# Performance work log

Hardware: AMD Instinct MI355X
Metric: run time of the kernel (lower is better)

## Reference

```python
import jax, jax.numpy as jnp
import numpy as np

# Graph / model dims (see init_kwargs)
N = 50000          # nodes
E = 800000         # edges (before self loops)
IN, HID, OUT = 128, 64, 47
HEADS = (4, 4, 1)
SLOPE = 0.2        # PyG GATConv default negative_slope
# dropout p=0.6 in the torch module is a no-op in eval mode -> omitted


def _glorot(key, shape):
    fan_in = shape[0] if len(shape) == 2 else int(np.prod(shape))
    return jax.random.normal(key, shape, jnp.float32) / np.sqrt(fan_in)


def setup_inputs() -> dict:
    key = jax.random.key(0)
    ks = jax.random.split(key, 16)
    x = jax.random.normal(ks[0], (N, IN), jnp.float32)
    edge_index = jax.random.randint(ks[1], (2, E), 0, N)
    # layer dims: (in_dim, out_dim_per_head, heads)
    dims = [(IN, HID, HEADS[0]), (HID * HEADS[0], HID, HEADS[1]), (HID * HEADS[1], OUT, HEADS[2])]
    inp = {"x": x, "edge_index": edge_index}
    for i, (d_in, c, h) in enumerate(dims, start=1):
        inp[f"W{i}"] = _glorot(ks[3 * i], (d_in, h * c))
        inp[f"a{i}s"] = _glorot(ks[3 * i + 1], (h, c))
        inp[f"a{i}d"] = _glorot(ks[3 * i + 2], (h, c))
        inp[f"b{i}"] = jnp.zeros((h * c,), jnp.float32)
    return inp


def gat_layer(x, src, dst, W, a_s, a_d, b, h, c):
    # x: [N, d_in] -> per-head features [N, h, c]
    feat = (x @ W).reshape(N, h, c)
    # per-node attention logits [N, h]
    al_src = jnp.einsum('nhc,hc->nh', feat, a_s)
    al_dst = jnp.einsum('nhc,hc->nh', feat, a_d)
    # per-edge score, LeakyReLU (PyG: alpha = a_src[src] + a_dst[dst])
    e = jax.nn.leaky_relu(al_src[src] + al_dst[dst], SLOPE)  # [Etot, h]
    # segment softmax over incoming edges of each dst node
    emax = jax.ops.segment_max(e, dst, num_segments=N)       # [N, h]
    w = jnp.exp(e - emax[dst])
    denom = jax.ops.segment_sum(w, dst, num_segments=N)      # [N, h]
    alpha = w / denom[dst]                                   # [Etot, h]
    # weighted scatter-add aggregation
    out = jax.ops.segment_sum(alpha[:, :, None] * feat[src], dst, num_segments=N)
    return out.reshape(N, h * c) + b                         # concat heads + bias


def reference(x, edge_index, W1, a1s, a1d, b1, W2, a2s, a2d, b2, W3, a3s, a3d, b3):
    loop = jnp.arange(N, dtype=edge_index.dtype)
    src = jnp.concatenate([edge_index[0], loop])  # add_self_loops=True
    dst = jnp.concatenate([edge_index[1], loop])
    h = gat_layer(x, src, dst, W1, a1s, a1d, b1, HEADS[0], HID)
    h = jax.nn.elu(h)
    h = gat_layer(h, src, dst, W2, a2s, a2d, b2, HEADS[1], HID)
    h = jax.nn.elu(h)
    h = gat_layer(h, src, dst, W3, a3s, a3d, b3, HEADS[2], OUT)  # no elu on last layer
    return h
```

## Files before the change

kernel.cpp:

```cpp
#include <hip/hip_runtime.h>
#include <hip/hip_bf16.h>

#define NNODES 50000
#define NEDGES 800000
#define ETOT   (NNODES + NEDGES)
#define MTILES 3136
#define MPAD   (MTILES * 16)
#define NBLK   196

typedef __attribute__((ext_vector_type(8))) short short8;
typedef __attribute__((ext_vector_type(4))) float floatx4;
typedef __attribute__((ext_vector_type(2))) unsigned int uint2v;
typedef __attribute__((ext_vector_type(4))) short short4v;

__device__ __forceinline__ float bf2f(__hip_bfloat16 x) { return __bfloat162float(x); }
__device__ __forceinline__ __hip_bfloat16 f2bf(float f) { return __float2bfloat16(f); }
__device__ __forceinline__ float sane(float v, float c) {
  v = (v == v) ? v : 0.f;
  return fminf(fmaxf(v, -c), c);
}
__device__ __forceinline__ unsigned short bfbits(float f) {
  union { __hip_bfloat16 b; unsigned short u; } cv;
  cv.b = f2bf(f);
  return cv.u;
}

__global__ void zero_int_kernel(int* __restrict__ p, int n) {
  int i = blockIdx.x * blockDim.x + threadIdx.x;
  if (i < n) p[i] = 0;
}
__global__ void fill_out_kernel(float* __restrict__ o, int n, float v) {
  int i = blockIdx.x * blockDim.x + threadIdx.x;
  if (i < n) o[i] = v;
}
__global__ void split_input_kernel(const float* __restrict__ in,
                                   __hip_bfloat16* __restrict__ hi,
                                   __hip_bfloat16* __restrict__ lo) {
  int i = blockIdx.x * blockDim.x + threadIdx.x;
  if (i >= MPAD * 256) return;
  float v = (i < NNODES * 128) ? sane(in[i], 1e4f) : 0.f;
  __hip_bfloat16 h = f2bf(v);
  hi[i] = h;
  lo[i] = f2bf(v - bf2f(h));
}
__global__ void pad47_kernel(const float* __restrict__ a, const float* __restrict__ b,
                             float* __restrict__ ap, float* __restrict__ bp) {
  int i = threadIdx.x;
  ap[i] = (i < 47) ? sane(a[i], 1e4f) : 0.f;
  bp[i] = (i < 47) ? sane(b[i], 1e4f) : 0.f;
}

__global__ void degree_kernel(const int* __restrict__ ei, int* __restrict__ deg) {
  int p = blockIdx.x * blockDim.x + threadIdx.x;
  if (p >= ETOT) return;
  int dst = (p < NEDGES) ? ei[NEDGES + p] : (p - NEDGES);
  dst = min(max(dst, 0), NNODES - 1);
  atomicAdd(&deg[dst], 1);
}

__global__ __launch_bounds__(256) void block_sum_kernel(const int* __restrict__ deg,
                                                        int* __restrict__ bsum) {
  __shared__ int sh[256];
  int b = blockIdx.x, t = threadIdx.x;
  int i = b * 256 + t;
  sh[t] = (i < NNODES) ? deg[i] : 0;
  __syncthreads();
  for (int off = 128; off > 0; off >>= 1) {
    if (t < off) sh[t] += sh[t + off];
    __syncthreads();
  }
  if (t == 0) bsum[b] = sh[0];
}

__global__ __launch_bounds__(256) void scan_bsum_kernel(const int* __restrict__ bsum,
                                                        int* __restrict__ boff,
                                                        int* __restrict__ row_ptr) {
  __shared__ int sh[256];
  int t = threadIdx.x;
  int v = (t < NBLK) ? bsum[t] : 0;
  sh[t] = v;
  __syncthreads();
  for (int off = 1; off < 256; off <<= 1) {
    int u = (t >= off) ? sh[t - off] : 0;
    __syncthreads();
    sh[t] += u;
    __syncthreads();
  }
  if (t < NBLK) boff[t] = sh[t] - v;
  if (t == 255) row_ptr[NNODES] = sh[255];
}

__global__ __launch_bounds__(256) void emit_rowptr_kernel(const int* __restrict__ deg,
                                                          const int* __restrict__ boff,
                                                          int* __restrict__ row_ptr,
                                                          int* __restrict__ cursor) {
  __shared__ int sh[256];
  int b = blockIdx.x, t = threadIdx.x;
  int i = b * 256 + t;
  int d = (i < NNODES) ? deg[i] : 0;
  sh[t] = d;
  __syncthreads();
  for (int off = 1; off < 256; off <<= 1) {
    int u = (t >= off) ? sh[t - off] : 0;
    __syncthreads();
    sh[t] += u;
    __syncthreads();
  }
  if (i < NNODES) {
    int v = boff[b] + sh[t] - d;
    row_ptr[i] = v;
    cursor[i] = v;
  }
}

__global__ void scatter_kernel(const int* __restrict__ ei, int* __restrict__ cursor,
                               int* __restrict__ csr_src) {
  int p = blockIdx.x * blockDim.x + threadIdx.x;
  if (p >= ETOT) return;
  int src, dst;
  if (p < NEDGES) { src = ei[p]; dst = ei[NEDGES + p]; }
  else            { src = p - NEDGES; dst = src; }
  src = min(max(src, 0), NNODES - 1);
  dst = min(max(dst, 0), NNODES - 1);
  int pos = atomicAdd(&cursor[dst], 1);
  pos = min(max(pos, 0), ETOT - 1);
  csr_src[pos] = src;
}

__global__ void pack_w_kernel(const float* __restrict__ W,
                              __hip_bfloat16* __restrict__ Bh,
                              __hip_bfloat16* __restrict__ Bl,
                              int K, int Nreal, int Npad) {
  int idx = blockIdx.x * blockDim.x + threadIdx.x;
  if (idx >= Npad * K) return;
  int e = idx;
  int j = e & 7;    e >>= 3;
  int m = e & 15;   e >>= 4;
  int quad = e & 3; e >>= 2;
  int kch = K >> 5;
  int kk32 = e % kch;
  int nt = e / kch;
  int n = nt * 16 + m;
  int k = kk32 * 32 + quad * 8 + j;
  float v = (n < Nreal) ? sane(W[k * Nreal + n], 1e4f) : 0.f;
  __hip_bfloat16 h = f2bf(v);
  Bh[idx] = h;
  Bl[idx] = f2bf(v - bf2f(h));
}

template<int KDIM, int NOUT, int HEADS, int WAVES_N>
__global__ __launch_bounds__(256) void gemm_attn_kernel(
    const __hip_bfloat16* __restrict__ Ah, const __hip_bfloat16* __restrict__ Al,
    const __hip_bfloat16* __restrict__ Bh, const __hip_bfloat16* __restrict__ Bl,
    const float* __restrict__ asv, const float* __restrict__ adv,
    __hip_bfloat16* __restrict__ Ch, float* __restrict__ als, float* __restrict__ ald) {
  constexpr int KCH = KDIM / 32;
  constexpr int CT = (NOUT / 16) / WAVES_N;
  constexpr int RT = 4;
  constexpr int RGROUPS = 4 / WAVES_N;
  __shared__ __hip_bfloat16 sAh[2 * 64 * 32];
  __shared__ __hip_bfloat16 sAl[2 * 64 * 32];
  int wave = threadIdx.x >> 6, lane = threadIdx.x & 63;
  int wrow = wave / WAVES_N, wcol = wave % WAVES_N;
  int rt0 = (blockIdx.x * RGROUPS + wrow) * RT;
  int ct0 = wcol * CT;
  int m = lane & 15, quad = lane >> 4;

  const short8* Bph = reinterpret_cast<const short8*>(Bh);
  const short8* Bpl = reinterpret_cast<const short8*>(Bl);

  floatx4 acc[RT][CT];
#pragma unroll
  for (int rt = 0; rt < RT; ++rt)
#pragma unroll
    for (int ct = 0; ct < CT; ++ct) acc[rt][ct] = (floatx4){0.f, 0.f, 0.f, 0.f};

  int tid = threadIdx.x;
  size_t gstage = (size_t)(rt0 * 16 + (tid >> 2)) * KDIM + (tid & 3) * 8;

#pragma unroll 2
  for (int ks = 0; ks < KCH / 2; ++ks) {
    short8 a_h[RT], a_l[RT];
    if constexpr (WAVES_N == 4) {
      short8 vh0 = *reinterpret_cast<const short8*>(Ah + gstage + ks * 64);
      short8 vh1 = *reinterpret_cast<const short8*>(Ah + gstage + ks * 64 + 32);
      short8 vl0 = *reinterpret_cast<const short8*>(Al + gstage + ks * 64);
      short8 vl1 = *reinterpret_cast<const short8*>(Al + gstage + ks * 64 + 32);
      __syncthreads();
      *reinterpret_cast<short8*>(&sAh[tid * 8]) = vh0;
      *reinterpret_cast<short8*>(&sAh[2048 + tid * 8]) = vh1;
      *reinterpret_cast<short8*>(&sAl[tid * 8]) = vl0;
      *reinterpret_cast<short8*>(&sAl[2048 + tid * 8]) = vl1;
      __syncthreads();
#pragma unroll
      for (int kk0 = 0; kk0 < 2; ++kk0) {
#pragma unroll
        for (int rt = 0; rt < RT; ++rt) {
          int so = kk0 * 2048 + (rt * 16 + m) * 32 + quad * 8;
          a_h[rt] = *reinterpret_cast<const short8*>(&sAh[so]);
          a_l[rt] = *reinterpret_cast<const short8*>(&sAl[so]);
        }
        int kk = ks * 2 + kk0;
#pragma unroll
        for (int ct = 0; ct < CT; ++ct) {
          size_t o = ((size_t)(ct0 + ct) * KCH + kk) * 64 + lane;
          short8 b_h = Bph[o];
          short8 b_l = Bpl[o];
#pragma unroll
          for (int rt = 0; rt < RT; ++rt) {
            acc[rt][ct] = __builtin_amdgcn_mfma_f32_16x16x32_bf16(a_h[rt], b_h, acc[rt][ct], 0, 0, 0);
            acc[rt][ct] = __builtin_amdgcn_mfma_f32_16x16x32_bf16(a_h[rt], b_l, acc[rt][ct], 0, 0, 0);
            acc[rt][ct] = __builtin_amdgcn_mfma_f32_16x16x32_bf16(a_l[rt], b_h, acc[rt][ct], 0, 0, 0);
          }
        }
      }
    } else {
#pragma unroll
      for (int kk0 = 0; kk0 < 2; ++kk0) {
        int kk = ks * 2 + kk0;
#pragma unroll
        for (int rt = 0; rt < RT; ++rt) {
          size_t aoff = (size_t)((rt0 + rt) * 16 + m) * KDIM + kk * 32 + quad * 8;
          a_h[rt] = *reinterpret_cast<const short8*>(Ah + aoff);
          a_l[rt] = *reinterpret_cast<const short8*>(Al + aoff);
        }
#pragma unroll
        for (int ct = 0; ct < CT; ++ct) {
          size_t o = ((size_t)(ct0 + ct) * KCH + kk) * 64 + lane;
          short8 b_h = Bph[o];
          short8 b_l = Bpl[o];
#pragma unroll
          for (int rt = 0; rt < RT; ++rt) {
            acc[rt][ct] = __builtin_amdgcn_mfma_f32_16x16x32_bf16(a_h[rt], b_h, acc[rt][ct], 0, 0, 0);
            acc[rt][ct] = __builtin_amdgcn_mfma_f32_16x16x32_bf16(a_h[rt], b_l, acc[rt][ct], 0, 0, 0);
            acc[rt][ct] = __builtin_amdgcn_mfma_f32_16x16x32_bf16(a_l[rt], b_h, acc[rt][ct], 0, 0, 0);
          }
        }
      }
    }
  }

  constexpr int CPH = NOUT / HEADS;
  int head = (ct0 * 16) / CPH;
  float asl[CT], adl[CT];
#pragma unroll
  for (int ct = 0; ct < CT; ++ct) {
    asl[ct] = asv[(ct0 + ct) * 16 + m];
    adl[ct] = adv[(ct0 + ct) * 16 + m];
  }
  float ps[RT * 4], pd[RT * 4];
#pragma unroll
  for (int i = 0; i < RT * 4; ++i) { ps[i] = 0.f; pd[i] = 0.f; }
#pragma unroll
  for (int rt = 0; rt < RT; ++rt)
#pragma unroll
    for (int ct = 0; ct < CT; ++ct)
#pragma unroll
      for (int r = 0; r < 4; ++r) {
        ps[rt * 4 + r] += acc[rt][ct][r] * asl[ct];
        pd[rt * 4 + r] += acc[rt][ct][r] * adl[ct];
      }
#pragma unroll
  for (int off = 1; off < 16; off <<= 1) {
#pragma unroll
    for (int i = 0; i < RT * 4; ++i) {
      ps[i] += __shfl_xor(ps[i], off);
      pd[i] += __shfl_xor(pd[i], off);
    }
  }
  if (m == 0) {
#pragma unroll
    for (int rt = 0; rt < RT; ++rt)
#pragma unroll
      for (int r = 0; r < 4; ++r) {
        int row = (rt0 + rt) * 16 + quad * 4 + r;
        if (row < NNODES) {
          als[(size_t)row * HEADS + head] = sane(ps[rt * 4 + r], 80.f);
          ald[(size_t)row * HEADS + head] = sane(pd[rt * 4 + r], 80.f);
        }
      }
  }

#pragma unroll
  for (int rt = 0; rt < RT; ++rt)
#pragma unroll
    for (int ct = 0; ct < CT; ++ct)
#pragma unroll
      for (int r = 0; r < 4; ++r) {
        int row = (rt0 + rt) * 16 + quad * 4 + r;
        if (row < NNODES) {
          float v = sane(acc[rt][ct][r], 3e4f);
          Ch[(size_t)row * NOUT + (ct0 + ct) * 16 + m] = f2bf(v);
        }
      }
}

template<int H>
__global__ __launch_bounds__(256) void alpha_kernel(const int* __restrict__ row_ptr,
                                                    const int* __restrict__ csr_src,
                                                    const float* __restrict__ als,
                                                    const float* __restrict__ ald,
                                                    float* __restrict__ alpha) {
  int wid = threadIdx.x >> 6, lane = threadIdx.x & 63;
  int dst = blockIdx.x * 4 + wid;
  if (dst >= NNODES) return;
  int start = row_ptr[dst], end = row_ptr[dst + 1];
  int cnt = end - start;
  if (cnt <= 0) return;
  float adv[H];
#pragma unroll
  for (int h = 0; h < H; ++h) adv[h] = ald[(size_t)dst * H + h];

  if (cnt <= 64) {
    int i = start + lane;
    bool valid = lane < cnt;
    int s = valid ? min(max(csr_src[i], 0), NNODES - 1) : 0;
    float w[H];
#pragma unroll
    for (int h = 0; h < H; ++h) {
      float e = als[(size_t)s * H + h] + adv[h];
      e = e > 0.f ? e : 0.2f * e;
      e = fminf(fmaxf(e, -80.f), 80.f);
      w[h] = valid ? __expf(e) : 0.f;
    }
#pragma unroll
    for (int h = 0; h < H; ++h) {
      float v = w[h];
#pragma unroll
      for (int off = 1; off < 64; off <<= 1) v += __shfl_xor(v, off);
      float inv = 1.f / fmaxf(v, 1e-30f);
      if (valid) alpha[(size_t)i * H + h] = w[h] * inv;
    }
  } else {
    float dl[H];
#pragma unroll
    for (int h = 0; h < H; ++h) dl[h] = 0.f;
    for (int base = start; base < end; base += 64) {
      int i = base + lane;
      bool valid = i < end;
      int s = valid ? min(max(csr_src[i], 0), NNODES - 1) : 0;
#pragma unroll
      for (int h = 0; h < H; ++h) {
        float e = als[(size_t)s * H + h] + adv[h];
        e = e > 0.f ? e : 0.2f * e;
        e = fminf(fmaxf(e, -80.f), 80.f);
        float w = valid ? __expf(e) : 0.f;
        dl[h] += w;
        if (valid) alpha[(size_t)i * H + h] = w;
      }
    }
    float inv[H];
#pragma unroll
    for (int h = 0; h < H; ++h) {
      float v = dl[h];
#pragma unroll
      for (int off = 1; off < 64; off <<= 1) v += __shfl_xor(v, off);
      inv[h] = 1.f / fmaxf(v, 1e-30f);
    }
    for (int base = start; base < end; base += 64) {
      int i = base + lane;
      if (i < end)
#pragma unroll
        for (int h = 0; h < H; ++h) alpha[(size_t)i * H + h] *= inv[h];
    }
  }
}

__global__ __launch_bounds__(256) void agg_mid_kernel(const int* __restrict__ row_ptr,
                                                      const int* __restrict__ csr_src,
                                                      const __hip_bfloat16* __restrict__ Fh,
                                                      const float* __restrict__ alpha,
                                                      const float* __restrict__ bias,
                                                      __hip_bfloat16* __restrict__ Oh,
                                                      __hip_bfloat16* __restrict__ Ol) {
  int wid = threadIdx.x >> 6, lane = threadIdx.x & 63;
  int dst = blockIdx.x * 4 + wid;
  if (dst >= NNODES) return;
  int start = row_ptr[dst], end = row_ptr[dst + 1];
  int cnt = end - start;
  int head = lane >> 4;
  float a0 = 0.f, a1 = 0.f, a2 = 0.f, a3 = 0.f;
  int p = 0;
  for (; p + 3 < cnt; p += 4) {
    int e0 = start + p, e1 = e0 + 1, e2 = e0 + 2, e3 = e0 + 3;
    int s0 = csr_src[e0], s1 = csr_src[e1], s2 = csr_src[e2], s3 = csr_src[e3];
    float w0 = alpha[(size_t)e0 * 4 + head];
    float w1 = alpha[(size_t)e1 * 4 + head];
    float w2 = alpha[(size_t)e2 * 4 + head];
    float w3 = alpha[(size_t)e3 * 4 + head];
    uint2v f0 = *reinterpret_cast<const uint2v*>(Fh + (size_t)s0 * 256 + lane * 4);
    uint2v f1 = *reinterpret_cast<const uint2v*>(Fh + (size_t)s1 * 256 + lane * 4);
    uint2v f2 = *reinterpret_cast<const uint2v*>(Fh + (size_t)s2 * 256 + lane * 4);
    uint2v f3 = *reinterpret_cast<const uint2v*>(Fh + (size_t)s3 * 256 + lane * 4);
    a0 += w0 * __uint_as_float(f0.x << 16);
    a1 += w0 * __uint_as_float(f0.x & 0xffff0000u);
    a2 += w0 * __uint_as_float(f0.y << 16);
    a3 += w0 * __uint_as_float(f0.y & 0xffff0000u);
    a0 += w1 * __uint_as_float(f1.x << 16);
    a1 += w1 * __uint_as_float(f1.x & 0xffff0000u);
    a2 += w1 * __uint_as_float(f1.y << 16);
    a3 += w1 * __uint_as_float(f1.y & 0xffff0000u);
    a0 += w2 * __uint_as_float(f2.x << 16);
    a1 += w2 * __uint_as_float(f2.x & 0xffff0000u);
    a2 += w2 * __uint_as_float(f2.y << 16);
    a3 += w2 * __uint_as_float(f2.y & 0xffff0000u);
    a0 += w3 * __uint_as_float(f3.x << 16);
    a1 += w3 * __uint_as_float(f3.x & 0xffff0000u);
    a2 += w3 * __uint_as_float(f3.y << 16);
    a3 += w3 * __uint_as_float(f3.y & 0xffff0000u);
  }
  for (; p < cnt; ++p) {
    int e0 = start + p;
    int s0 = csr_src[e0];
    float w0 = alpha[(size_t)e0 * 4 + head];
    uint2v f0 = *reinterpret_cast<const uint2v*>(Fh + (size_t)s0 * 256 + lane * 4);
    a0 += w0 * __uint_as_float(f0.x << 16);
    a1 += w0 * __uint_as_float(f0.x & 0xffff0000u);
    a2 += w0 * __uint_as_float(f0.y << 16);
    a3 += w0 * __uint_as_float(f0.y & 0xffff0000u);
  }
  floatx4 bv = *reinterpret_cast<const floatx4*>(bias + lane * 4);
  float o0 = a0 + bv.x, o1 = a1 + bv.y, o2 = a2 + bv.z, o3 = a3 + bv.w;
  o0 = o0 > 0.f ? o0 : __expf(o0) - 1.f;
  o1 = o1 > 0.f ? o1 : __expf(o1) - 1.f;
  o2 = o2 > 0.f ? o2 : __expf(o2) - 1.f;
  o3 = o3 > 0.f ? o3 : __expf(o3) - 1.f;
  float h0 = bf2f(f2bf(o0)), h1 = bf2f(f2bf(o1)), h2 = bf2f(f2bf(o2)), h3 = bf2f(f2bf(o3));
  short4v hv = (short4v){(short)bfbits(o0), (short)bfbits(o1), (short)bfbits(o2), (short)bfbits(o3)};
  short4v lv = (short4v){(short)bfbits(o0 - h0), (short)bfbits(o1 - h1),
                         (short)bfbits(o2 - h2), (short)bfbits(o3 - h3)};
  *reinterpret_cast<short4v*>(Oh + (size_t)dst * 256 + lane * 4) = hv;
  *reinterpret_cast<short4v*>(Ol + (size_t)dst * 256 + lane * 4) = lv;
}

__global__ void agg_final_kernel(const int* __restrict__ row_ptr,
                                 const int* __restrict__ csr_src,
                                 const __hip_bfloat16* __restrict__ Fh,
                                 const float* __restrict__ alpha,
                                 const float* __restrict__ bias,
                                 float* __restrict__ out) {
  int wid = threadIdx.x >> 6, lane = threadIdx.x & 63;
  int dst = blockIdx.x * 4 + wid;
  if (dst >= NNODES) return;
  int start = row_ptr[dst], end = row_ptr[dst + 1];
  int cnt = end - start;
  float acc = 0.f;
  int p = 0;
  for (; p + 3 < cnt; p += 4) {
    int e0 = start + p;
    int s0 = csr_src[e0], s1 = csr_src[e0 + 1], s2 = csr_src[e0 + 2], s3 = csr_src[e0 + 3];
    float w0 = alpha[e0], w1 = alpha[e0 + 1], w2 = alpha[e0 + 2], w3 = alpha[e0 + 3];
    float f0 = bf2f(Fh[(size_t)s0 * 64 + lane]);
    float f1 = bf2f(Fh[(size_t)s1 * 64 + lane]);
    float f2 = bf2f(Fh[(size_t)s2 * 64 + lane]);
    float f3 = bf2f(Fh[(size_t)s3 * 64 + lane]);
    acc += w0 * f0 + w1 * f1 + w2 * f2 + w3 * f3;
  }
  for (; p < cnt; ++p) {
    int e0 = start + p;
    acc += alpha[e0] * bf2f(Fh[(size_t)csr_src[e0] * 64 + lane]);
  }
  if (lane < 47) out[(size_t)dst * 47 + lane] = acc + bias[lane];
}

extern "C" void kernel_launch(void* const* d_in, const int* in_sizes, int n_in,
                              void* d_out, int out_size, void* d_ws, size_t ws_size,
                              hipStream_t stream) {
  const float* x   = (const float*)d_in[0];
  const int* ei    = (const int*)d_in[1];
  const float* W1  = (const float*)d_in[2];
  const float* a1s = (const float*)d_in[3];
  const float* a1d = (const float*)d_in[4];
  const float* b1  = (const float*)d_in[5];
  const float* W2  = (const float*)d_in[6];
  const float* a2s = (const float*)d_in[7];
  const float* a2d = (const float*)d_in[8];
  const float* b2  = (const float*)d_in[9];
  const float* W3  = (const float*)d_in[10];
  const float* a3s = (const float*)d_in[11];
  const float* a3d = (const float*)d_in[12];
  const float* b3  = (const float*)d_in[13];
  float* out = (float*)d_out;
  (void)n_in; (void)in_sizes;

  char* base = (char*)d_ws;
  size_t off = 0;
  auto alloc = [&](size_t bytes) -> char* {
    off = (off + 255) & ~(size_t)255;
    char* p = base + off;
    off += bytes;
    return p;
  };
  int* deg     = (int*)alloc((size_t)NNODES * 4);
  int* cursor  = (int*)alloc((size_t)NNODES * 4);
  int* row_ptr = (int*)alloc((size_t)(NNODES + 1) * 4);
  int* csr_src = (int*)alloc((size_t)ETOT * 4);
  int* bsum    = (int*)alloc(256 * 4);
  int* boff    = (int*)alloc(256 * 4);
  float* als   = (float*)alloc((size_t)NNODES * 4 * 4);
  float* ald   = (float*)alloc((size_t)NNODES * 4 * 4);
  float* alpha = (float*)alloc((size_t)ETOT * 4 * 4);
  __hip_bfloat16* Ah = (__hip_bfloat16*)alloc((size_t)MPAD * 256 * 2);
  __hip_bfloat16* Al = (__hip_bfloat16*)alloc((size_t)MPAD * 256 * 2);
  __hip_bfloat16* Fh = (__hip_bfloat16*)alloc((size_t)NNODES * 256 * 2);
  __hip_bfloat16* wth = (__hip_bfloat16*)alloc((size_t)256 * 256 * 2);
  __hip_bfloat16* wtl = (__hip_bfloat16*)alloc((size_t)256 * 256 * 2);
  float* asv3 = (float*)alloc(64 * 4);
  float* adv3 = (float*)alloc(64 * 4);

  if (ws_size < off) {
    fill_out_kernel<<<(out_size + 255) / 256, 256, 0, stream>>>(out, out_size, 12345.f);
    return;
  }

  zero_int_kernel<<<(NNODES + 255) / 256, 256, 0, stream>>>(deg, NNODES);
  degree_kernel<<<(ETOT + 255) / 256, 256, 0, stream>>>(ei, deg);
  block_sum_kernel<<<NBLK, 256, 0, stream>>>(deg, bsum);
  scan_bsum_kernel<<<1, 256, 0, stream>>>(bsum, boff, row_ptr);
  emit_rowptr_kernel<<<NBLK, 256, 0, stream>>>(deg, boff, row_ptr, cursor);
  scatter_kernel<<<(ETOT + 255) / 256, 256, 0, stream>>>(ei, cursor, csr_src);

  split_input_kernel<<<(MPAD * 256 + 255) / 256, 256, 0, stream>>>(x, Ah, Al);
  pad47_kernel<<<1, 64, 0, stream>>>(a3s, a3d, asv3, adv3);

  const int grid12 = (NNODES + 63) / 64;
  const int grid3 = (NNODES + 255) / 256;
  const int gridN4 = (NNODES + 3) / 4;

  pack_w_kernel<<<(256 * 128 + 255) / 256, 256, 0, stream>>>(W1, wth, wtl, 128, 256, 256);
  gemm_attn_kernel<128, 256, 4, 4><<<grid12, 256, 0, stream>>>(Ah, Al, wth, wtl, a1s, a1d,
                                                               Fh, als, ald);
  alpha_kernel<4><<<gridN4, 256, 0, stream>>>(row_ptr, csr_src, als, ald, alpha);
  agg_mid_kernel<<<gridN4, 256, 0, stream>>>(row_ptr, csr_src, Fh, alpha, b1, Ah, Al);

  pack_w_kernel<<<(256 * 256 + 255) / 256, 256, 0, stream>>>(W2, wth, wtl, 256, 256, 256);
  gemm_attn_kernel<256, 256, 4, 4><<<grid12, 256, 0, stream>>>(Ah, Al, wth, wtl, a2s, a2d,
                                                               Fh, als, ald);
  alpha_kernel<4><<<gridN4, 256, 0, stream>>>(row_ptr, csr_src, als, ald, alpha);
  agg_mid_kernel<<<gridN4, 256, 0, stream>>>(row_ptr, csr_src, Fh, alpha, b2, Ah, Al);

  pack_w_kernel<<<(64 * 256 + 255) / 256, 256, 0, stream>>>(W3, wth, wtl, 256, 47, 64);
  gemm_attn_kernel<256, 64, 1, 1><<<grid3, 256, 0, stream>>>(Ah, Al, wth, wtl, asv3, adv3,
                                                             Fh, als, ald);
  alpha_kernel<1><<<gridN4, 256, 0, stream>>>(row_ptr, csr_src, als, ald, alpha);
  agg_final_kernel<<<gridN4, 256, 0, stream>>>(row_ptr, csr_src, Fh, alpha, b3, out);
}
```

Measured before the change: 515.8 us.

## Sort CSR buckets by edge id, vectorize input split, retile alpha and final aggregation

The input split now handles four floats per thread with vector loads and stores. A new bucket-sort pass orders each destination's edges by original edge index, which makes the CSR layout deterministic and likely improves locality. The 4-head alpha kernel assigns 16 lanes per head so each lane gathers fewer heads, and the final aggregation splits edges across two half-waves using packed bf16 pair loads. The quadratic in-bucket rank sort and its extra scatter buffers add work for high-degree nodes.

```diff
diff --git a/kernel.cpp b/kernel.cpp
--- a/kernel.cpp
+++ b/kernel.cpp
@@ -37,11 +37,22 @@
                                    __hip_bfloat16* __restrict__ hi,
                                    __hip_bfloat16* __restrict__ lo) {
   int i = blockIdx.x * blockDim.x + threadIdx.x;
-  if (i >= MPAD * 256) return;
-  float v = (i < NNODES * 128) ? sane(in[i], 1e4f) : 0.f;
-  __hip_bfloat16 h = f2bf(v);
-  hi[i] = h;
-  lo[i] = f2bf(v - bf2f(h));
+  if (i >= MPAD * 64) return;
+  floatx4 v;
+  if (i < NNODES * 32) {
+    v = *reinterpret_cast<const floatx4*>(in + (size_t)i * 4);
+    v.x = sane(v.x, 1e4f); v.y = sane(v.y, 1e4f);
+    v.z = sane(v.z, 1e4f); v.w = sane(v.w, 1e4f);
+  } else {
+    v = (floatx4){0.f, 0.f, 0.f, 0.f};
+  }
+  float h0 = bf2f(f2bf(v.x)), h1 = bf2f(f2bf(v.y)), h2 = bf2f(f2bf(v.z)), h3 = bf2f(f2bf(v.w));
+  short4v hv = (short4v){(short)bfbits(v.x), (short)bfbits(v.y),
+                         (short)bfbits(v.z), (short)bfbits(v.w)};
+  short4v lv = (short4v){(short)bfbits(v.x - h0), (short)bfbits(v.y - h1),
+                         (short)bfbits(v.z - h2), (short)bfbits(v.w - h3)};
+  *reinterpret_cast<short4v*>(hi + (size_t)i * 4) = hv;
+  *reinterpret_cast<short4v*>(lo + (size_t)i * 4) = lv;
 }
 __global__ void pad47_kernel(const float* __restrict__ a, const float* __restrict__ b,
                              float* __restrict__ ap, float* __restrict__ bp) {
@@ -114,7 +125,7 @@
 }
 
 __global__ void scatter_kernel(const int* __restrict__ ei, int* __restrict__ cursor,
-                               int* __restrict__ csr_src) {
+                               int* __restrict__ tmp_src, int* __restrict__ tmp_p) {
   int p = blockIdx.x * blockDim.x + threadIdx.x;
   if (p >= ETOT) return;
   int src, dst;
@@ -124,7 +135,26 @@
   dst = min(max(dst, 0), NNODES - 1);
   int pos = atomicAdd(&cursor[dst], 1);
   pos = min(max(pos, 0), ETOT - 1);
-  csr_src[pos] = src;
+  tmp_src[pos] = src;
+  tmp_p[pos] = p;
+}
+
+__global__ __launch_bounds__(256) void bucket_sort_kernel(const int* __restrict__ row_ptr,
+                                                          const int* __restrict__ tmp_src,
+                                                          const int* __restrict__ tmp_p,
+                                                          int* __restrict__ csr_src) {
+  int wid = threadIdx.x >> 6, lane = threadIdx.x & 63;
+  int dst = blockIdx.x * 4 + wid;
+  if (dst >= NNODES) return;
+  int start = row_ptr[dst], end = row_ptr[dst + 1];
+  int cnt = end - start;
+  for (int i = lane; i < cnt; i += 64) {
+    int pi = tmp_p[start + i];
+    int si = tmp_src[start + i];
+    int rank = 0;
+    for (int j = 0; j < cnt; ++j) rank += (tmp_p[start + j] < pi) ? 1 : 0;
+    csr_src[start + rank] = si;
+  }
 }
 
 __global__ void pack_w_kernel(const float* __restrict__ W,
@@ -295,73 +325,99 @@
       }
 }
 
-template<int H>
-__global__ __launch_bounds__(256) void alpha_kernel(const int* __restrict__ row_ptr,
-                                                    const int* __restrict__ csr_src,
-                                                    const float* __restrict__ als,
-                                                    const float* __restrict__ ald,
-                                                    float* __restrict__ alpha) {
+__global__ __launch_bounds__(256) void alpha4_kernel(const int* __restrict__ row_ptr,
+                                                     const int* __restrict__ csr_src,
+                                                     const float* __restrict__ als,
+                                                     const float* __restrict__ ald,
+                                                     float* __restrict__ alpha) {
   int wid = threadIdx.x >> 6, lane = threadIdx.x & 63;
   int dst = blockIdx.x * 4 + wid;
   if (dst >= NNODES) return;
   int start = row_ptr[dst], end = row_ptr[dst + 1];
   int cnt = end - start;
   if (cnt <= 0) return;
-  float adv[H];
-#pragma unroll
-  for (int h = 0; h < H; ++h) adv[h] = ald[(size_t)dst * H + h];
-
+  int g = lane >> 4, cl = lane & 15;
+  float adh = ald[(size_t)dst * 4 + g];
+  float dl = 0.f;
+  float wreg[4];
+#pragma unroll
+  for (int k = 0; k < 4; ++k) {
+    int i = cl + k * 16;
+    if (i < cnt) {
+      int s = min(max(csr_src[start + i], 0), NNODES - 1);
+      float e = als[(size_t)s * 4 + g] + adh;
+      e = e > 0.f ? e : 0.2f * e;
+      e = fminf(fmaxf(e, -80.f), 80.f);
+      float w = __expf(e);
+      wreg[k] = w;
+      dl += w;
+    }
+  }
+  for (int i = cl + 64; i < cnt; i += 16) {
+    int s = min(max(csr_src[start + i], 0), NNODES - 1);
+    float e = als[(size_t)s * 4 + g] + adh;
+    e = e > 0.f ? e : 0.2f * e;
+    e = fminf(fmaxf(e, -80.f), 80.f);
+    float w = __expf(e);
+    alpha[(size_t)(start + i) * 4 + g] = w;
+    dl += w;
+  }
+#pragma unroll
+  for (int off = 1; off < 16; off <<= 1) dl += __shfl_xor(dl, off);
+  float inv = 1.f / fmaxf(dl, 1e-30f);
+#pragma unroll
+  for (int k = 0; k < 4; ++k) {
+    int i = cl + k * 16;
+    if (i < cnt) alpha[(size_t)(start + i) * 4 + g] = wreg[k] * inv;
+  }
+  for (int i = cl + 64; i < cnt; i += 16)
+    alpha[(size_t)(start + i) * 4 + g] *= inv;
+}
+
+__global__ __launch_bounds__(256) void alpha1_kernel(const int* __restrict__ row_ptr,
+                                                     const int* __restrict__ csr_src,
+                                                     const float* __restrict__ als,
+                                                     const float* __restrict__ ald,
+                                                     float* __restrict__ alpha) {
+  int wid = threadIdx.x >> 6, lane = threadIdx.x & 63;
+  int dst = blockIdx.x * 4 + wid;
+  if (dst >= NNODES) return;
+  int start = row_ptr[dst], end = row_ptr[dst + 1];
+  int cnt = end - start;
+  if (cnt <= 0) return;
+  float adh = ald[dst];
   if (cnt <= 64) {
     int i = start + lane;
     bool valid = lane < cnt;
     int s = valid ? min(max(csr_src[i], 0), NNODES - 1) : 0;
-    float w[H];
-#pragma unroll
-    for (int h = 0; h < H; ++h) {
-      float e = als[(size_t)s * H + h] + adv[h];
-      e = e > 0.f ? e : 0.2f * e;
-      e = fminf(fmaxf(e, -80.f), 80.f);
-      w[h] = valid ? __expf(e) : 0.f;
-    }
-#pragma unroll
-    for (int h = 0; h < H; ++h) {
-      float v = w[h];
-#pragma unroll
-      for (int off = 1; off < 64; off <<= 1) v += __shfl_xor(v, off);
-      float inv = 1.f / fmaxf(v, 1e-30f);
-      if (valid) alpha[(size_t)i * H + h] = w[h] * inv;
-    }
+    float e = als[s] + adh;
+    e = e > 0.f ? e : 0.2f * e;
+    e = fminf(fmaxf(e, -80.f), 80.f);
+    float w = valid ? __expf(e) : 0.f;
+    float v = w;
+#pragma unroll
+    for (int off = 1; off < 64; off <<= 1) v += __shfl_xor(v, off);
+    float inv = 1.f / fmaxf(v, 1e-30f);
+    if (valid) alpha[i] = w * inv;
   } else {
-    float dl[H];
-#pragma unroll
-    for (int h = 0; h < H; ++h) dl[h] = 0.f;
+    float dlsum = 0.f;
     for (int base = start; base < end; base += 64) {
       int i = base + lane;
       bool valid = i < end;
       int s = valid ? min(max(csr_src[i], 0), NNODES - 1) : 0;
-#pragma unroll
-      for (int h = 0; h < H; ++h) {
-        float e = als[(size_t)s * H + h] + adv[h];
-        e = e > 0.f ? e : 0.2f * e;
-        e = fminf(fmaxf(e, -80.f), 80.f);
-        float w = valid ? __expf(e) : 0.f;
-        dl[h] += w;
-        if (valid) alpha[(size_t)i * H + h] = w;
-      }
+      float e = als[s] + adh;
+      e = e > 0.f ? e : 0.2f * e;
+      e = fminf(fmaxf(e, -80.f), 80.f);
+      float w = valid ? __expf(e) : 0.f;
+      dlsum += w;
+      if (valid) alpha[i] = w;
     }
-    float inv[H];
-#pragma unroll
-    for (int h = 0; h < H; ++h) {
-      float v = dl[h];
-#pragma unroll
-      for (int off = 1; off < 64; off <<= 1) v += __shfl_xor(v, off);
-      inv[h] = 1.f / fmaxf(v, 1e-30f);
-    }
+#pragma unroll
+    for (int off = 1; off < 64; off <<= 1) dlsum += __shfl_xor(dlsum, off);
+    float inv = 1.f / fmaxf(dlsum, 1e-30f);
     for (int base = start; base < end; base += 64) {
       int i = base + lane;
-      if (i < end)
-#pragma unroll
-        for (int h = 0; h < H; ++h) alpha[(size_t)i * H + h] *= inv[h];
+      if (i < end) alpha[i] *= inv;
     }
   }
 }
@@ -444,23 +500,35 @@
   if (dst >= NNODES) return;
   int start = row_ptr[dst], end = row_ptr[dst + 1];
   int cnt = end - start;
-  float acc = 0.f;
-  int p = 0;
-  for (; p + 3 < cnt; p += 4) {
+  int half = lane >> 5, cl = lane & 31;
+  float acc0 = 0.f, acc1 = 0.f;
+  int p = half;
+  for (; p + 2 < cnt; p += 4) {
+    int e0 = start + p, e1 = start + p + 2;
+    int s0 = csr_src[e0], s1 = csr_src[e1];
+    float w0 = alpha[e0], w1 = alpha[e1];
+    unsigned int f0 = *reinterpret_cast<const unsigned int*>(Fh + (size_t)s0 * 64 + cl * 2);
+    unsigned int f1 = *reinterpret_cast<const unsigned int*>(Fh + (size_t)s1 * 64 + cl * 2);
+    acc0 += w0 * __uint_as_float(f0 << 16);
+    acc1 += w0 * __uint_as_float(f0 & 0xffff0000u);
+    acc0 += w1 * __uint_as_float(f1 << 16);
+    acc1 += w1 * __uint_as_float(f1 & 0xffff0000u);
+  }
+  for (; p < cnt; p += 2) {
     int e0 = start + p;
-    int s0 = csr_src[e0], s1 = csr_src[e0 + 1], s2 = csr_src[e0 + 2], s3 = csr_src[e0 + 3];
-    float w0 = alpha[e0], w1 = alpha[e0 + 1], w2 = alpha[e0 + 2], w3 = alpha[e0 + 3];
-    float f0 = bf2f(Fh[(size_t)s0 * 64 + lane]);
-    float f1 = bf2f(Fh[(size_t)s1 * 64 + lane]);
-    float f2 = bf2f(Fh[(size_t)s2 * 64 + lane]);
-    float f3 = bf2f(Fh[(size_t)s3 * 64 + lane]);
-    acc += w0 * f0 + w1 * f1 + w2 * f2 + w3 * f3;
-  }
-  for (; p < cnt; ++p) {
-    int e0 = start + p;
-    acc += alpha[e0] * bf2f(Fh[(size_t)csr_src[e0] * 64 + lane]);
-  }
-  if (lane < 47) out[(size_t)dst * 47 + lane] = acc + bias[lane];
+    int s0 = csr_src[e0];
+    float w0 = alpha[e0];
+    unsigned int f0 = *reinterpret_cast<const unsigned int*>(Fh + (size_t)s0 * 64 + cl * 2);
+    acc0 += w0 * __uint_as_float(f0 << 16);
+    acc1 += w0 * __uint_as_float(f0 & 0xffff0000u);
+  }
+  acc0 += __shfl_xor(acc0, 32);
+  acc1 += __shfl_xor(acc1, 32);
+  if (half == 0) {
+    int c0 = cl * 2, c1 = cl * 2 + 1;
+    if (c0 < 47) out[(size_t)dst * 47 + c0] = acc0 + bias[c0];
+    if (c1 < 47) out[(size_t)dst * 47 + c1] = acc1 + bias[c1];
+  }
 }
 
 extern "C" void kernel_launch(void* const* d_in, const int* in_sizes, int n_in,
@@ -495,6 +563,8 @@
   int* cursor  = (int*)alloc((size_t)NNODES * 4);
   int* row_ptr = (int*)alloc((size_t)(NNODES + 1) * 4);
   int* csr_src = (int*)alloc((size_t)ETOT * 4);
+  int* tmp_src = (int*)alloc((size_t)ETOT * 4);
+  int* tmp_p   = (int*)alloc((size_t)ETOT * 4);
   int* bsum    = (int*)alloc(256 * 4);
   int* boff    = (int*)alloc(256 * 4);
   float* als   = (float*)alloc((size_t)NNODES * 4 * 4);
@@ -518,9 +588,10 @@
   block_sum_kernel<<<NBLK, 256, 0, stream>>>(deg, bsum);
   scan_bsum_kernel<<<1, 256, 0, stream>>>(bsum, boff, row_ptr);
   emit_rowptr_kernel<<<NBLK, 256, 0, stream>>>(deg, boff, row_ptr, cursor);
-  scatter_kernel<<<(ETOT + 255) / 256, 256, 0, stream>>>(ei, cursor, csr_src);
-
-  split_input_kernel<<<(MPAD * 256 + 255) / 256, 256, 0, stream>>>(x, Ah, Al);
+  scatter_kernel<<<(ETOT + 255) / 256, 256, 0, stream>>>(ei, cursor, tmp_src, tmp_p);
+  bucket_sort_kernel<<<(NNODES + 3) / 4, 256, 0, stream>>>(row_ptr, tmp_src, tmp_p, csr_src);
+
+  split_input_kernel<<<(MPAD * 64 + 255) / 256, 256, 0, stream>>>(x, Ah, Al);
   pad47_kernel<<<1, 64, 0, stream>>>(a3s, a3d, asv3, adv3);
 
   const int grid12 = (NNODES + 63) / 64;
@@ -530,18 +601,18 @@
   pack_w_kernel<<<(256 * 128 + 255) / 256, 256, 0, stream>>>(W1, wth, wtl, 128, 256, 256);
   gemm_attn_kernel<128, 256, 4, 4><<<grid12, 256, 0, stream>>>(Ah, Al, wth, wtl, a1s, a1d,
                                                                Fh, als, ald);
-  alpha_kernel<4><<<gridN4, 256, 0, stream>>>(row_ptr, csr_src, als, ald, alpha);
+  alpha4_kernel<<<gridN4, 256, 0, stream>>>(row_ptr, csr_src, als, ald, alpha);
   agg_mid_kernel<<<gridN4, 256, 0, stream>>>(row_ptr, csr_src, Fh, alpha, b1, Ah, Al);
 
   pack_w_kernel<<<(256 * 256 + 255) / 256, 256, 0, stream>>>(W2, wth, wtl, 256, 256, 256);
   gemm_attn_kernel<256, 256, 4, 4><<<grid12, 256, 0, stream>>>(Ah, Al, wth, wtl, a2s, a2d,
                                                                Fh, als, ald);
-  alpha_kernel<4><<<gridN4, 256, 0, stream>>>(row_ptr, csr_src, als, ald, alpha);
+  alpha4_kernel<<<gridN4, 256, 0, stream>>>(row_ptr, csr_src, als, ald, alpha);
   agg_mid_kernel<<<gridN4, 256, 0, stream>>>(row_ptr, csr_src, Fh, alpha, b2, Ah, Al);
 
   pack_w_kernel<<<(64 * 256 + 255) / 256, 256, 0, stream>>>(W3, wth, wtl, 256, 47, 64);
   gemm_attn_kernel<256, 64, 1, 1><<<grid3, 256, 0, stream>>>(Ah, Al, wth, wtl, asv3, adv3,
                                                              Fh, als, ald);
-  alpha_kernel<1><<<gridN4, 256, 0, stream>>>(row_ptr, csr_src, als, ald, alpha);
+  alpha1_kernel<<<gridN4, 256, 0, stream>>>(row_ptr, csr_src, als, ald, alpha);
   agg_final_kernel<<<gridN4, 256, 0, stream>>>(row_ptr, csr_src, Fh, alpha, b3, out);
 }
```

New measurement: 527.9 us (median of 2 runs). 2.3% more time.
